# Optimization experiments

Hardware: AMD Instinct MI355X
Metric: run time of the kernel (lower is better)

The kernel has to match this reference:

```python
import jax, jax.numpy as jnp
import numpy as np

DIM, HEADS, WS = 256, 16, 8
B, H, W = 2, 252, 252
BN_EPS = 1e-5


def _rel_index():
    # Same construction as the torch buffer relative_position_index (64,64)
    coords = np.stack(np.meshgrid(np.arange(WS), np.arange(WS), indexing='ij'))
    flat = coords.reshape(2, -1)
    rel = (flat[:, :, None] - flat[:, None, :]).transpose(1, 2, 0).copy()
    rel[..., 0] += WS - 1
    rel[..., 1] += WS - 1
    rel[..., 0] *= 2 * WS - 1
    return jnp.asarray(rel.sum(-1))

REL_IDX = _rel_index()  # (WS*WS, WS*WS) int


def _conv(x, w, pad, groups=1):
    return jax.lax.conv_general_dilated(
        x, w, (1, 1), [(pad[0], pad[0]), (pad[1], pad[1])],
        dimension_numbers=('NCHW', 'OIHW', 'NCHW'), feature_group_count=groups)


def setup_inputs() -> dict:
    key = jax.random.key(0)
    ks = jax.random.split(key, 8)
    s = lambda k, shape, sc: jax.random.normal(k, shape, jnp.float32) * sc
    z = lambda: jnp.zeros((DIM,), jnp.float32)
    return {
        'x': s(ks[0], (B, DIM, H, W), 1.0),
        'w_qkv': s(ks[1], (3 * DIM, DIM, 1, 1), 0.05),
        'rel_bias_table': s(ks[2], ((2 * WS - 1) ** 2, HEADS), 0.02),
        'w_h': s(ks[3], (DIM, DIM, WS, 1), 0.02),
        'b_h': z(),
        'w_v': s(ks[4], (DIM, DIM, 1, WS), 0.02),
        'b_v': z(),
        'w_dw': s(ks[5], (DIM, 1, WS, WS), 0.05),
        'bn_gamma': jnp.ones((DIM,), jnp.float32),
        'bn_beta': z(),
        'bn_mean': z(),
        'bn_var': jnp.ones((DIM,), jnp.float32),
        'w_pw': s(ks[6], (DIM, DIM, 1, 1), 0.05),
    }


def reference(x, w_qkv, rel_bias_table, w_h, b_h, w_v, b_v, w_dw,
              bn_gamma, bn_beta, bn_mean, bn_var, w_pw):
    Bc, C, Hc, Wc = x.shape
    pad_h, pad_w = WS - Hc % WS, WS - Wc % WS
    xp = jnp.pad(x, ((0, 0), (0, 0), (0, pad_h), (0, pad_w)), mode='reflect')
    Hp, Wp = Hc + pad_h, Wc + pad_w
    hh, ww, d = Hp // WS, Wp // WS, C // HEADS

    qkv = _conv(xp, w_qkv, (0, 0))  # (B, 3C, Hp, Wp)
    # b (qkv h d) (hh ws1) (ww ws2) -> qkv (b hh ww) h (ws1 ws2) d
    qkv = qkv.reshape(Bc, 3, HEADS, d, hh, WS, ww, WS)
    qkv = qkv.transpose(1, 0, 4, 6, 2, 5, 7, 3).reshape(3, Bc * hh * ww, HEADS, WS * WS, d)
    q, k, v = qkv[0], qkv[1], qkv[2]

    dots = jnp.einsum('nhid,nhjd->nhij', q, k) * (d ** -0.5)
    bias = rel_bias_table[REL_IDX.reshape(-1)].reshape(WS * WS, WS * WS, HEADS)
    dots = dots + bias.transpose(2, 0, 1)[None]  # (1, h, 64, 64)
    attn = jax.nn.softmax(dots, axis=-1)
    out = jnp.einsum('nhij,nhjd->nhid', attn, v)
    # (b hh ww) h (ws1 ws2) d -> b (h d) (hh ws1) (ww ws2)
    out = out.reshape(Bc, hh, ww, HEADS, WS, WS, d)
    out = out.transpose(0, 3, 6, 1, 4, 2, 5).reshape(Bc, C, Hp, Wp)
    out = out[:, :, :Hc, :Wc]

    p1 = _conv(jnp.pad(out, ((0, 0), (0, 0), (0, 1), (0, 0)), mode='reflect'),
               w_h, (WS // 2 - 1, 0)) + b_h[None, :, None, None]
    p2 = _conv(jnp.pad(out, ((0, 0), (0, 0), (0, 0), (0, 1)), mode='reflect'),
               w_v, (0, WS // 2 - 1)) + b_v[None, :, None, None]
    y = jnp.pad(p1 + p2, ((0, 0), (0, 0), (0, 1), (0, 1)), mode='reflect')
    y = _conv(y, w_dw, ((WS - 1) // 2, (WS - 1) // 2), groups=DIM)  # depthwise
    inv = bn_gamma / jnp.sqrt(bn_var + BN_EPS)
    y = y * inv[None, :, None, None] + (bn_beta - bn_mean * inv)[None, :, None, None]
    y = _conv(y, w_pw, (0, 0))  # pointwise 1x1
    return y[:, :, :Hc, :Wc]
```

## Files before the change

### kernel.cpp

```cpp
#include <hip/hip_runtime.h>
#include <hip/hip_bf16.h>

#define HC 252
#define WC 252
#define CD 256
#define NHEADS 16

#define XP_W 264
#define XP_ROW (XP_W*256)
#define XP_BH  (252*XP_ROW)

typedef unsigned short u16;
typedef unsigned int u32;
typedef __attribute__((ext_vector_type(8))) short bf16x8;
typedef __attribute__((ext_vector_type(4))) float f32x4;
typedef __attribute__((ext_vector_type(4))) u32 u32x4;
typedef __attribute__((ext_vector_type(2))) u32 u32x2;

#define XP_BYTES (2u * 2u * (unsigned)XP_BH)
#define ZP_OFF   XP_BYTES
#define ZP_BYTES 409600u
#define WT_OFF   (ZP_OFF + ZP_BYTES)
#define WT_ELEMS (128*8192)
#define WPW_OFF  (WT_OFF + (unsigned)WT_ELEMS*2u)
#define WPW_ELEMS (8*8192)
#define WQ_OFF   (WPW_OFF + (unsigned)WPW_ELEMS*2u)
#define WQ_ELEMS (768*256)
#define BIAS_OFF (WQ_OFF + (unsigned)WQ_ELEMS*2u)

__device__ __forceinline__ u16 bfu(float f) {
    __hip_bfloat16 h = __float2bfloat16(f);
    return *(reinterpret_cast<u16*>(&h));
}
__device__ __forceinline__ u32 pack2(float a, float b) {
    return (u32)bfu(a) | ((u32)bfu(b) << 16);
}
__device__ __forceinline__ float bf2f(u16 v) {
    union { u32 u; float f; } cv; cv.u = ((u32)v) << 16; return cv.f;
}

__global__ __launch_bounds__(256, 2) void attn_mfma(
    const float* __restrict__ x, const u16* __restrict__ WQ,
    const float* __restrict__ BIASF, u16* __restrict__ xp)
{
    __shared__ __align__(16) char smem[73728];

    const int bid = blockIdx.x;
    const int zz = (bid & 7) * 256 + (bid >> 3);
    const int wx = zz & 31, wy = (zz >> 5) & 31, b = zz >> 10;
    const int tid = threadIdx.x;
    const int lane = tid & 63, wid = tid >> 6;
    const int g = lane >> 4, li = lane & 15;

    {
        int ci = tid;
        const float* srcc = x + (size_t)(b * 256 + ci) * (HC * WC);
        #pragma unroll
        for (int r = 0; r < 8; ++r) {
            int h = wy * 8 + r; if (h >= HC) h = 2 * HC - 2 - h;
            const float* src = srcc + h * WC;
            float v[8];
            if (wx == 31) {
                #pragma unroll
                for (int c = 0; c < 8; ++c) {
                    int w = 248 + c; if (w >= WC) w = 2 * WC - 2 - w;
                    v[c] = src[w];
                }
            } else {
                float4 f0 = *(const float4*)(src + wx * 8);
                float4 f1 = *(const float4*)(src + wx * 8 + 4);
                v[0]=f0.x; v[1]=f0.y; v[2]=f0.z; v[3]=f0.w;
                v[4]=f1.x; v[5]=f1.y; v[6]=f1.z; v[7]=f1.w;
            }
            #pragma unroll
            for (int c = 0; c < 8; ++c) {
                int pos = r * 8 + c;
                int byte = pos * 512 + ((ci * 2) ^ ((pos & 7) << 4));
                *(u16*)(smem + byte) = bfu(v[c]);
            }
        }
    }
    __syncthreads();

    const int WB = 32768 + wid * 10240;
    char* Qb = smem + WB;
    char* Kb = smem + WB + 2048;
    char* Vb = smem + WB + 4096;
    char* Pb = smem + WB + 6144;

    const bf16x8 zf = {0,0,0,0,0,0,0,0};

    #pragma unroll 1
    for (int hh = 0; hh < 4; ++hh) {
        const int head = wid * 4 + hh;

        f32x4 acc[3][4];
        #pragma unroll
        for (int p = 0; p < 3; ++p)
            #pragma unroll
            for (int nf = 0; nf < 4; ++nf) acc[p][nf] = (f32x4){0.f,0.f,0.f,0.f};

        for (int ks = 0; ks < 8; ++ks) {
            bf16x8 bx[4];
            #pragma unroll
            for (int nf = 0; nf < 4; ++nf) {
                int pos = 16 * nf + li;
                int byte = pos * 512 + ((ks * 64 + 16 * g) ^ ((pos & 7) << 4));
                bx[nf] = *(const bf16x8*)(smem + byte);
            }
            bf16x8 aw[3];
            #pragma unroll
            for (int p = 0; p < 3; ++p) {
                int o = p * 256 + head * 16 + li;
                aw[p] = *(const bf16x8*)(WQ + o * 256 + ks * 32 + 8 * g);
            }
            __builtin_amdgcn_s_setprio(1);
            #pragma unroll
            for (int p = 0; p < 3; ++p)
                #pragma unroll
                for (int nf = 0; nf < 4; ++nf)
                    acc[p][nf] = __builtin_amdgcn_mfma_f32_16x16x32_bf16(aw[p], bx[nf], acc[p][nf], 0, 0, 0);
            __builtin_amdgcn_s_setprio(0);
        }

        #pragma unroll
        for (int p = 0; p < 3; ++p) {
            if (p < 2) {
                char* base = (p == 0) ? Qb : Kb;
                #pragma unroll
                for (int nf = 0; nf < 4; ++nf) {
                    int pos = 16 * nf + li;
                    u32 lo = pack2(acc[p][nf][0], acc[p][nf][1]);
                    u32 hi = pack2(acc[p][nf][2], acc[p][nf][3]);
                    int byte = pos * 32 + ((8 * g) ^ (((pos >> 2) & 1) << 4));
                    *(u32x2*)(base + byte) = (u32x2){lo, hi};
                }
            } else {
                #pragma unroll
                for (int nf = 0; nf < 4; ++nf) {
                    int pos = 16 * nf + li;
                    #pragma unroll
                    for (int r = 0; r < 4; ++r) {
                        int d = 4 * g + r;
                        int byte = (pos >> 3) * 256 + d * 16 + (pos & 7) * 2;
                        *(u16*)(Vb + byte) = bfu(acc[p][nf][r]);
                    }
                }
            }
        }

        f32x4 s[4][4];
        #pragma unroll
        for (int mf = 0; mf < 4; ++mf)
            #pragma unroll
            for (int nf = 0; nf < 4; ++nf) s[mf][nf] = (f32x4){0.f,0.f,0.f,0.f};
        bf16x8 bk[4];
        #pragma unroll
        for (int nf = 0; nf < 4; ++nf) {
            int pos = 16 * nf + li;
            bk[nf] = (g < 2) ? *(const bf16x8*)(Kb + pos * 32 + ((16 * g) ^ (((pos >> 2) & 1) << 4))) : zf;
        }
        __builtin_amdgcn_s_setprio(1);
        #pragma unroll
        for (int mf = 0; mf < 4; ++mf) {
            int pos = 16 * mf + li;
            bf16x8 aq = (g < 2) ? *(const bf16x8*)(Qb + pos * 32 + ((16 * g) ^ (((pos >> 2) & 1) << 4))) : zf;
            #pragma unroll
            for (int nf = 0; nf < 4; ++nf)
                s[mf][nf] = __builtin_amdgcn_mfma_f32_16x16x32_bf16(aq, bk[nf], s[mf][nf], 0, 0, 0);
        }
        __builtin_amdgcn_s_setprio(0);

        f32x4 e[4][4];
        f32x4 rs[4];
        #pragma unroll
        for (int mf = 0; mf < 4; ++mf) rs[mf] = (f32x4){0.f,0.f,0.f,0.f};
        #pragma unroll
        for (int mf = 0; mf < 4; ++mf)
            #pragma unroll
            for (int nf = 0; nf < 4; ++nf) {
                f32x4 b4 = *(const f32x4*)(BIASF + (((head * 4 + mf) * 4 + nf) * 64 + lane) * 4);
                #pragma unroll
                for (int r = 0; r < 4; ++r) {
                    float ev = __expf(s[mf][nf][r] * 0.25f + b4[r]);
                    e[mf][nf][r] = ev;
                    rs[mf][r] += ev;
                }
            }
        #pragma unroll
        for (int mf = 0; mf < 4; ++mf)
            #pragma unroll
            for (int r = 0; r < 4; ++r) {
                float t = rs[mf][r];
                t += __shfl_xor(t, 1); t += __shfl_xor(t, 2);
                t += __shfl_xor(t, 4); t += __shfl_xor(t, 8);
                rs[mf][r] = t;
            }

        f32x4 o[4];
        #pragma unroll
        for (int mf = 0; mf < 4; ++mf) o[mf] = (f32x4){0.f,0.f,0.f,0.f};
        const bool even = !(lane & 1);
        #pragma unroll
        for (int hf = 0; hf < 2; ++hf) {
            #pragma unroll
            for (int mf = 0; mf < 4; ++mf)
                #pragma unroll
                for (int nfl = 0; nfl < 2; ++nfl) {
                    f32x4 ee = e[mf][2 * hf + nfl];
                    float p0 = __shfl_xor(ee[0], 1), p1 = __shfl_xor(ee[1], 1);
                    float p2 = __shfl_xor(ee[2], 1), p3 = __shfl_xor(ee[3], 1);
                    int jl = 16 * nfl + (li & ~1);
                    u32 w0, w1; int r0;
                    if (even) { w0 = pack2(ee[0], p0); w1 = pack2(ee[1], p1); r0 = 0; }
                    else      { w0 = pack2(p2, ee[2]); w1 = pack2(p3, ee[3]); r0 = 2; }
                    int i0 = 16 * mf + 4 * g + r0, i1 = i0 + 1;
                    *(u32*)(Pb + i0 * 64 + ((2 * jl) ^ ((i0 & 3) << 4))) = w0;
                    *(u32*)(Pb + i1 * 64 + ((2 * jl) ^ ((i1 & 3) << 4))) = w1;
                }
            bf16x8 bv = *(const bf16x8*)(Vb + (4 * hf + g) * 256 + li * 16);
            __builtin_amdgcn_s_setprio(1);
            #pragma unroll
            for (int mf = 0; mf < 4; ++mf) {
                int i = 16 * mf + li;
                bf16x8 ap = *(const bf16x8*)(Pb + i * 64 + ((16 * g) ^ ((i & 3) << 4)));
                o[mf] = __builtin_amdgcn_mfma_f32_16x16x32_bf16(ap, bv, o[mf], 0, 0, 0);
            }
            __builtin_amdgcn_s_setprio(0);
        }

        #pragma unroll
        for (int mf = 0; mf < 4; ++mf) {
            int h = wy * 8 + 2 * mf + (g >> 1);
            int wbase = wx * 8 + 4 * (g & 1);
            if (h < HC && wbase < WC) {
                size_t rowb = ((size_t)(b * HC + h)) * XP_ROW + (size_t)(head * 16 + li);
                #pragma unroll
                for (int r = 0; r < 4; ++r) {
                    float v = o[mf][r] / rs[mf][r];
                    xp[rowb + (size_t)(wbase + r + 4) * 256] = bfu(v);
                }
            }
        }
    }
}

__global__ __launch_bounds__(256) void wprep_kernel(
    const float* __restrict__ wh, const float* __restrict__ wv,
    const float* __restrict__ wpw, const float* __restrict__ wqkv,
    const float* __restrict__ btab, u16* __restrict__ wsu)
{
    int i = blockIdx.x * 256 + threadIdx.x;
    u16* WT = wsu + WT_OFF / 2;
    u16* WP = wsu + WPW_OFF / 2;
    u16* ZP = wsu + ZP_OFF / 2;
    u16* WQp = wsu + WQ_OFF / 2;
    float* BF = (float*)(wsu + BIAS_OFF / 2);
    if (i < WT_ELEMS) {
        int j = i & 7, l = (i >> 3) & 1023, s = i >> 13;
        int kb = (l >> 8) & 3;
        int co = (l & 255) ^ (kb << 1);
        float v;
        if (s < 64) {
            int t = s >> 3, ci = (s & 7) * 32 + kb * 8 + j;
            v = wh[co * 2048 + ci * 8 + t];
        } else {
            int s2 = s - 64;
            int t = s2 >> 3, ci = (s2 & 7) * 32 + kb * 8 + j;
            v = wv[co * 2048 + ci * 8 + t];
        }
        WT[i] = bfu(v);
    } else if (i < WT_ELEMS + WPW_ELEMS) {
        int i2 = i - WT_ELEMS;
        int j = i2 & 7, l = (i2 >> 3) & 1023, s = i2 >> 13;
        int kb = (l >> 8) & 3;
        int co = (l & 255) ^ (kb << 1);
        WP[i2] = bfu(wpw[co * 256 + s * 32 + kb * 8 + j]);
    } else if (i < WT_ELEMS + WPW_ELEMS + (int)(ZP_BYTES / 2)) {
        ZP[i - WT_ELEMS - WPW_ELEMS] = 0;
    } else if (i < WT_ELEMS + WPW_ELEMS + (int)(ZP_BYTES / 2) + WQ_ELEMS) {
        int i4 = i - WT_ELEMS - WPW_ELEMS - (int)(ZP_BYTES / 2);
        WQp[i4] = bfu(wqkv[i4]);
    } else {
        int i5 = i - WT_ELEMS - WPW_ELEMS - (int)(ZP_BYTES / 2) - WQ_ELEMS;
        if (i5 < 16384) {
            int lane = i5 & 63, nf = (i5 >> 6) & 3, mf = (i5 >> 8) & 3, head = i5 >> 10;
            int gg = lane >> 4, ll = lane & 15;
            #pragma unroll
            for (int r = 0; r < 4; ++r) {
                int row = 16 * mf + 4 * gg + r;
                int col = 16 * nf + ll;
                int dy = (row >> 3) - (col >> 3) + 7;
                int dx = (row & 7) - (col & 7) + 7;
                BF[i5 * 4 + r] = btab[(dy * 15 + dx) * NHEADS + head];
            }
        }
    }
}

__global__ __launch_bounds__(256) void halo_kernel(u16* __restrict__ xp)
{
    int i = blockIdx.x * 256 + threadIdx.x;
    if (i >= 2 * 252 * 12 * 256) return;
    int ci = i & 255;
    int c12 = (i >> 8) % 12;
    int row = i / (12 * 256);
    int wp = (c12 < 4) ? c12 : 252 + c12;
    u16 v = 0;
    if (wp == 256) v = xp[(size_t)row * XP_ROW + 254 * 256 + ci];
    xp[(size_t)row * XP_ROW + (size_t)wp * 256 + ci] = v;
}

__global__ __launch_bounds__(512, 2) void sepconv_mfma(
    const u16* __restrict__ xpt, const u16* __restrict__ WT,
    const u16* __restrict__ ZP,
    const float* __restrict__ b_h, const float* __restrict__ b_v,
    u16* __restrict__ P)
{
    __shared__ __align__(16) u16 As[2][8192];
    __shared__ __align__(16) u16 Bs[2][256 * 36];

    const int bid = blockIdx.x;
    const int zz = (bid & 7) * 63 + (bid >> 3);
    const int h = zz % HC, b = zz / HC;
    const int tid = threadIdx.x;
    const int lane = tid & 63, wid = tid >> 6;
    const int wr = wid >> 2, wc = wid & 3;
    const int cq = lane & 15, kb = lane >> 4;

    const int wB = tid & 255;
    const int oc0 = tid >> 8;
    const int tb = (wB + 4) * 256 + oc0 * 8;
    const int bsw = wB * 36 + oc0 * 8;

    const u16* const xb = xpt + (size_t)(b * HC) * XP_ROW;

    f32x4 acc[8][4];
    #pragma unroll
    for (int m = 0; m < 8; ++m)
        #pragma unroll
        for (int n = 0; n < 4; ++n) acc[m][n] = (f32x4){0.f, 0.f, 0.f, 0.f};

    u32x4 rA[2];
    u32x4 rB0, rB1;

#define SC_SRC(t, RP, SO)                                                      \
    if ((t) < 64) {                                                            \
        int tt = (t) >> 3;                                                     \
        int jt = h + tt - 3;                                                   \
        int jr = (jt == 252) ? 250 : jt;                                       \
        RP = (jt >= 0 && jt <= 252) ? (xpt + ((size_t)(b * HC) + jr) * XP_ROW) : ZP; \
        SO = ((t) & 7) * 32;                                                   \
    } else {                                                                   \
        int tt = ((t) - 64) >> 3;                                              \
        RP = xb + (size_t)h * XP_ROW + (tt - 3) * 256;                         \
        SO = (((t) - 64) & 7) * 32;                                            \
    }

    rA[0] = *(const u32x4*)(WT + (size_t)tid * 8);
    rA[1] = *(const u32x4*)(WT + (size_t)(512 + tid) * 8);
    {
        const u16* rp; int so;
        SC_SRC(0, rp, so)
        rB0 = *(const u32x4*)(rp + so + tb);
        rB1 = *(const u32x4*)(rp + so + tb + 16);
    }
    *(u32x4*)&As[0][(size_t)tid * 8] = rA[0];
    *(u32x4*)&As[0][(size_t)(512 + tid) * 8] = rA[1];
    *(u32x4*)&Bs[0][bsw] = rB0;
    *(u32x4*)&Bs[0][bsw + 16] = rB1;

    #pragma unroll 1
    for (int s = 0; s < 128; ++s) {
        const int cur = s & 1;
        const int s1 = s + 1;
        if (s1 < 128) {
            rA[0] = *(const u32x4*)(WT + (size_t)s1 * 8192 + (size_t)tid * 8);
            rA[1] = *(const u32x4*)(WT + (size_t)s1 * 8192 + (size_t)(512 + tid) * 8);
            const u16* rp; int so;
            SC_SRC(s1, rp, so)
            rB0 = *(const u32x4*)(rp + so + tb);
            rB1 = *(const u32x4*)(rp + so + tb + 16);
        }
        __syncthreads();

        {
            bf16x8 af[8], bfr[4];
            #pragma unroll
            for (int m = 0; m < 8; ++m) {
                int row = wr * 128 + m * 16 + cq;
                af[m] = *(const bf16x8*)&As[cur][(kb * 256 + (row ^ (kb << 1))) * 8];
            }
            #pragma unroll
            for (int n = 0; n < 4; ++n)
                bfr[n] = *(const bf16x8*)&Bs[cur][(wc * 64 + n * 16 + cq) * 36 + kb * 8];
            __builtin_amdgcn_s_setprio(1);
            #pragma unroll
            for (int m = 0; m < 8; ++m)
                #pragma unroll
                for (int n = 0; n < 4; ++n)
                    acc[m][n] = __builtin_amdgcn_mfma_f32_16x16x32_bf16(af[m], bfr[n], acc[m][n], 0, 0, 0);
            __builtin_amdgcn_s_setprio(0);
        }

        if (s1 < 128) {
            const int nxt = cur ^ 1;
            *(u32x4*)&As[nxt][(size_t)tid * 8] = rA[0];
            *(u32x4*)&As[nxt][(size_t)(512 + tid) * 8] = rA[1];
            *(u32x4*)&Bs[nxt][bsw] = rB0;
            *(u32x4*)&Bs[nxt][bsw + 16] = rB1;
        }
    }
#undef SC_SRC

    const int rq = lane >> 4, cc = lane & 15;
    #pragma unroll
    for (int m = 0; m < 8; ++m) {
        int cgb = wr * 128 + m * 16 + rq * 4;
        float bias[4];
        #pragma unroll
        for (int rr = 0; rr < 4; ++rr) bias[rr] = b_h[cgb + rr] + b_v[cgb + rr];
        #pragma unroll
        for (int n = 0; n < 4; ++n) {
            int wg = wc * 64 + n * 16 + cc;
            if (wg < WC) {
                #pragma unroll
                for (int rr = 0; rr < 4; ++rr)
                    P[((size_t)(b * CD + cgb + rr) * HC + h) * WC + wg] = bfu(acc[m][n][rr] + bias[rr]);
            }
        }
    }
}

__global__ __launch_bounds__(256) void dwbn_kernel(
    const u16* __restrict__ P, const float* __restrict__ w_dw,
    const float* __restrict__ gamma, const float* __restrict__ beta,
    const float* __restrict__ mean, const float* __restrict__ var,
    __hip_bfloat16* __restrict__ Yb)
{
    __shared__ float ps[15][42];
    __shared__ float wd[64];
    const int bw = blockIdx.x, bh = blockIdx.y, bz = blockIdx.z;
    const int b = bz >> 8, c = bz & 255;
    const int h0 = bh * 8, w0 = bw * 32;
    const int tid = threadIdx.x;
    if (tid < 64) wd[tid] = w_dw[c * 64 + tid];
    for (int it = 0; it < 3; ++it) {
        int flat = tid + it * 256;
        if (flat < 630) {
            int row = flat / 42, col = flat % 42;
            int j = h0 - 3 + row, wcol = w0 - 3 + col;
            float v = 0.f;
            if (j >= 0 && j <= HC && wcol >= 0 && wcol <= WC) {
                int jr = (j == HC) ? (HC - 2) : j;
                int wr2 = (wcol == WC) ? (WC - 2) : wcol;
                v = bf2f(P[((size_t)(b * CD + c) * HC + jr) * WC + wr2]);
            }
            ps[row][col] = v;
        }
    }
    __syncthreads();
    const int r = tid >> 5, cc = tid & 31;
    const int h = h0 + r, w = w0 + cc;
    if (h < HC && w < WC) {
        float s = 0.f;
        #pragma unroll
        for (int u = 0; u < 8; ++u)
            #pragma unroll
            for (int v2 = 0; v2 < 8; ++v2)
                s += wd[u * 8 + v2] * ps[r + u][cc + v2];
        const float inv = gamma[c] * rsqrtf(var[c] + 1e-5f);
        Yb[((b * CD + c) * HC + h) * WC + w] = __float2bfloat16(s * inv + (beta[c] - mean[c] * inv));
    }
}

__global__ __launch_bounds__(512, 2) void pw_mfma(
    const u16* __restrict__ Y, const u16* __restrict__ WP,
    float* __restrict__ O)
{
    __shared__ __align__(16) u16 As[2][8192];
    __shared__ __align__(16) u16 Bs[2][256 * 36];

    const int bid = blockIdx.x;
    const int zz = (bid & 7) * 63 + (bid >> 3);
    const int h = zz % HC, b = zz / HC;
    const int tid = threadIdx.x;
    const int lane = tid & 63, wid = tid >> 6;
    const int wr = wid >> 2, wc = wid & 3;
    const int cq = lane & 15, kb = lane >> 4;

    const int wl2 = (tid & 127) * 2;
    const int oc = tid >> 7;

    const u16* yb = Y + ((size_t)(b * 256 + oc * 8) * HC + h) * WC + wl2;

    const int bw0 = wl2 * 36 + oc * 8;
    const int bw1 = bw0 + 36;

    f32x4 acc[8][4];
    #pragma unroll
    for (int m = 0; m < 8; ++m)
        #pragma unroll
        for (int n = 0; n < 4; ++n) acc[m][n] = (f32x4){0.f, 0.f, 0.f, 0.f};

    u32x4 rA[2];
    u32 rB[8];

    rA[0] = *(const u32x4*)(WP + (size_t)tid * 8);
    rA[1] = *(const u32x4*)(WP + (size_t)(512 + tid) * 8);
    #pragma unroll
    for (int j = 0; j < 8; ++j)
        rB[j] = *(const u32*)(yb + (size_t)j * (HC * WC));
    *(u32x4*)&As[0][(size_t)tid * 8] = rA[0];
    *(u32x4*)&As[0][(size_t)(512 + tid) * 8] = rA[1];
    {
        union { bf16x8 v; u32 u[4]; } p0, p1;
        #pragma unroll
        for (int q = 0; q < 4; ++q) {
            p0.u[q] = __builtin_amdgcn_perm(rB[2 * q + 1], rB[2 * q], 0x05040100u);
            p1.u[q] = __builtin_amdgcn_perm(rB[2 * q + 1], rB[2 * q], 0x07060302u);
        }
        *(bf16x8*)&Bs[0][bw0] = p0.v;
        *(bf16x8*)&Bs[0][bw1] = p1.v;
    }

    #pragma unroll 1
    for (int s = 0; s < 8; ++s) {
        const int cur = s & 1;
        const int s1 = s + 1;
        if (s1 < 8) {
            rA[0] = *(const u32x4*)(WP + (size_t)s1 * 8192 + (size_t)tid * 8);
            rA[1] = *(const u32x4*)(WP + (size_t)s1 * 8192 + (size_t)(512 + tid) * 8);
            #pragma unroll
            for (int j = 0; j < 8; ++j)
                rB[j] = *(const u32*)(yb + (size_t)(s1 * 32 + j) * (HC * WC));
        }
        __syncthreads();

        {
            bf16x8 af[8], bfr[4];
            #pragma unroll
            for (int m = 0; m < 8; ++m) {
                int row = wr * 128 + m * 16 + cq;
                af[m] = *(const bf16x8*)&As[cur][(kb * 256 + (row ^ (kb << 1))) * 8];
            }
            #pragma unroll
            for (int n = 0; n < 4; ++n)
                bfr[n] = *(const bf16x8*)&Bs[cur][(wc * 64 + n * 16 + cq) * 36 + kb * 8];
            __builtin_amdgcn_s_setprio(1);
            #pragma unroll
            for (int m = 0; m < 8; ++m)
                #pragma unroll
                for (int n = 0; n < 4; ++n)
                    acc[m][n] = __builtin_amdgcn_mfma_f32_16x16x32_bf16(af[m], bfr[n], acc[m][n], 0, 0, 0);
            __builtin_amdgcn_s_setprio(0);
        }

        if (s1 < 8) {
            const int nxt = cur ^ 1;
            *(u32x4*)&As[nxt][(size_t)tid * 8] = rA[0];
            *(u32x4*)&As[nxt][(size_t)(512 + tid) * 8] = rA[1];
            union { bf16x8 v; u32 u[4]; } p0, p1;
            #pragma unroll
            for (int q = 0; q < 4; ++q) {
                p0.u[q] = __builtin_amdgcn_perm(rB[2 * q + 1], rB[2 * q], 0x05040100u);
                p1.u[q] = __builtin_amdgcn_perm(rB[2 * q + 1], rB[2 * q], 0x07060302u);
            }
            *(bf16x8*)&Bs[nxt][bw0] = p0.v;
            *(bf16x8*)&Bs[nxt][bw1] = p1.v;
        }
    }

    const int rq = lane >> 4, cc = lane & 15;
    #pragma unroll
    for (int m = 0; m < 8; ++m) {
        int cgb = wr * 128 + m * 16 + rq * 4;
        #pragma unroll
        for (int n = 0; n < 4; ++n) {
            int wg = wc * 64 + n * 16 + cc;
            if (wg < WC) {
                #pragma unroll
                for (int rr = 0; rr < 4; ++rr)
                    O[((size_t)(b * CD + cgb + rr) * HC + h) * WC + wg] = acc[m][n][rr];
            }
        }
    }
}

extern "C" void kernel_launch(void* const* d_in, const int* in_sizes, int n_in,
                              void* d_out, int out_size, void* d_ws, size_t ws_size,
                              hipStream_t stream)
{
    const float* x      = (const float*)d_in[0];
    const float* w_qkv  = (const float*)d_in[1];
    const float* bias_t = (const float*)d_in[2];
    const float* w_h    = (const float*)d_in[3];
    const float* b_h    = (const float*)d_in[4];
    const float* w_v    = (const float*)d_in[5];
    const float* b_v    = (const float*)d_in[6];
    const float* w_dw   = (const float*)d_in[7];
    const float* bn_g   = (const float*)d_in[8];
    const float* bn_b   = (const float*)d_in[9];
    const float* bn_m   = (const float*)d_in[10];
    const float* bn_v   = (const float*)d_in[11];
    const float* w_pw   = (const float*)d_in[12];
    float* out = (float*)d_out;

    u16* wsu = (u16*)d_ws;
    const u16* XPu = wsu;
    const u16* ZPu = wsu + ZP_OFF / 2;
    const u16* WTu = wsu + WT_OFF / 2;
    const u16* WPu = wsu + WPW_OFF / 2;
    const u16* WQu = wsu + WQ_OFF / 2;
    const float* BFu = (const float*)(wsu + BIAS_OFF / 2);

    wprep_kernel<<<5984, 256, 0, stream>>>(w_h, w_v, w_pw, w_qkv, bias_t, wsu);
    attn_mfma<<<2048, 256, 0, stream>>>(x, WQu, BFu, wsu);
    halo_kernel<<<6048, 256, 0, stream>>>(wsu);
    sepconv_mfma<<<504, 512, 0, stream>>>(XPu, WTu, ZPu, b_h, b_v, (u16*)d_out);
    dwbn_kernel<<<dim3(8, 32, 512), 256, 0, stream>>>((const u16*)d_out, w_dw, bn_g, bn_b,
                                                      bn_m, bn_v, (__hip_bfloat16*)d_ws);
    pw_mfma<<<504, 512, 0, stream>>>(wsu, WPu, out);
}
```

Measured before the change: 689.6 us.

## Software-pipeline QKV projection, enlarge depthwise tiles, stage pointwise output through LDS

The attention kernel now computes the next head's QKV projection while the current head's softmax and PV run, and drops the setprio hints. The depthwise+BN kernel handles 16x64 tiles with four outputs per thread and writes packed bf16 pairs, so halo loads are reused across more outputs and global stores are wider. The pointwise kernel transposes its accumulators through LDS so each lane writes float4 rows instead of scattered scalar stores. Together these target latency hiding and memory-store efficiency, at the cost of higher register pressure in the attention kernel (an extra 12 f32x4 accumulators) and an extra LDS round trip in the pointwise epilogue.

```diff
diff --git a/kernel.cpp b/kernel.cpp
--- a/kernel.cpp
+++ b/kernel.cpp
@@ -12,6 +12,7 @@
 
 typedef unsigned short u16;
 typedef unsigned int u32;
+typedef __attribute__((ext_vector_type(4))) u16 u16x4;
 typedef __attribute__((ext_vector_type(8))) short bf16x8;
 typedef __attribute__((ext_vector_type(4))) float f32x4;
 typedef __attribute__((ext_vector_type(4))) u32 u32x4;
@@ -90,39 +91,36 @@
 
     const bf16x8 zf = {0,0,0,0,0,0,0,0};
 
+#define QKV_LOOP(ACC, HEADV)                                                  \
+    for (int ks = 0; ks < 8; ++ks) {                                          \
+        bf16x8 bx[4];                                                         \
+        _Pragma("unroll") for (int nf = 0; nf < 4; ++nf) {                    \
+            int pos = 16 * nf + li;                                           \
+            int byte = pos * 512 + ((ks * 64 + 16 * g) ^ ((pos & 7) << 4));   \
+            bx[nf] = *(const bf16x8*)(smem + byte);                           \
+        }                                                                     \
+        bf16x8 aw[3];                                                         \
+        _Pragma("unroll") for (int p = 0; p < 3; ++p) {                       \
+            int o = p * 256 + (HEADV) * 16 + li;                              \
+            aw[p] = *(const bf16x8*)(WQ + o * 256 + ks * 32 + 8 * g);         \
+        }                                                                     \
+        _Pragma("unroll") for (int p = 0; p < 3; ++p) {                       \
+            _Pragma("unroll") for (int nf = 0; nf < 4; ++nf)                  \
+                ACC[p][nf] = __builtin_amdgcn_mfma_f32_16x16x32_bf16(aw[p], bx[nf], ACC[p][nf], 0, 0, 0); \
+        }                                                                     \
+    }
+
+    f32x4 accA[3][4], accN[3][4];
+    #pragma unroll
+    for (int p = 0; p < 3; ++p)
+        #pragma unroll
+        for (int nf = 0; nf < 4; ++nf) accA[p][nf] = (f32x4){0.f,0.f,0.f,0.f};
+    QKV_LOOP(accA, wid * 4)
+
     #pragma unroll 1
     for (int hh = 0; hh < 4; ++hh) {
         const int head = wid * 4 + hh;
 
-        f32x4 acc[3][4];
-        #pragma unroll
-        for (int p = 0; p < 3; ++p)
-            #pragma unroll
-            for (int nf = 0; nf < 4; ++nf) acc[p][nf] = (f32x4){0.f,0.f,0.f,0.f};
-
-        for (int ks = 0; ks < 8; ++ks) {
-            bf16x8 bx[4];
-            #pragma unroll
-            for (int nf = 0; nf < 4; ++nf) {
-                int pos = 16 * nf + li;
-                int byte = pos * 512 + ((ks * 64 + 16 * g) ^ ((pos & 7) << 4));
-                bx[nf] = *(const bf16x8*)(smem + byte);
-            }
-            bf16x8 aw[3];
-            #pragma unroll
-            for (int p = 0; p < 3; ++p) {
-                int o = p * 256 + head * 16 + li;
-                aw[p] = *(const bf16x8*)(WQ + o * 256 + ks * 32 + 8 * g);
-            }
-            __builtin_amdgcn_s_setprio(1);
-            #pragma unroll
-            for (int p = 0; p < 3; ++p)
-                #pragma unroll
-                for (int nf = 0; nf < 4; ++nf)
-                    acc[p][nf] = __builtin_amdgcn_mfma_f32_16x16x32_bf16(aw[p], bx[nf], acc[p][nf], 0, 0, 0);
-            __builtin_amdgcn_s_setprio(0);
-        }
-
         #pragma unroll
         for (int p = 0; p < 3; ++p) {
             if (p < 2) {
@@ -130,8 +128,8 @@
                 #pragma unroll
                 for (int nf = 0; nf < 4; ++nf) {
                     int pos = 16 * nf + li;
-                    u32 lo = pack2(acc[p][nf][0], acc[p][nf][1]);
-                    u32 hi = pack2(acc[p][nf][2], acc[p][nf][3]);
+                    u32 lo = pack2(accA[p][nf][0], accA[p][nf][1]);
+                    u32 hi = pack2(accA[p][nf][2], accA[p][nf][3]);
                     int byte = pos * 32 + ((8 * g) ^ (((pos >> 2) & 1) << 4));
                     *(u32x2*)(base + byte) = (u32x2){lo, hi};
                 }
@@ -143,7 +141,7 @@
                     for (int r = 0; r < 4; ++r) {
                         int d = 4 * g + r;
                         int byte = (pos >> 3) * 256 + d * 16 + (pos & 7) * 2;
-                        *(u16*)(Vb + byte) = bfu(acc[p][nf][r]);
+                        *(u16*)(Vb + byte) = bfu(accA[p][nf][r]);
                     }
                 }
             }
@@ -170,6 +168,14 @@
                 s[mf][nf] = __builtin_amdgcn_mfma_f32_16x16x32_bf16(aq, bk[nf], s[mf][nf], 0, 0, 0);
         }
         __builtin_amdgcn_s_setprio(0);
+
+        if (hh < 3) {
+            #pragma unroll
+            for (int p = 0; p < 3; ++p)
+                #pragma unroll
+                for (int nf = 0; nf < 4; ++nf) accN[p][nf] = (f32x4){0.f,0.f,0.f,0.f};
+            QKV_LOOP(accN, head + 1)
+        }
 
         f32x4 e[4][4];
         f32x4 rs[4];
@@ -242,7 +248,15 @@
                 }
             }
         }
-    }
+
+        if (hh < 3) {
+            #pragma unroll
+            for (int p = 0; p < 3; ++p)
+                #pragma unroll
+                for (int nf = 0; nf < 4; ++nf) accA[p][nf] = accN[p][nf];
+        }
+    }
+#undef QKV_LOOP
 }
 
 __global__ __launch_bounds__(256) void wprep_kernel(
@@ -438,17 +452,17 @@
     const float* __restrict__ mean, const float* __restrict__ var,
     __hip_bfloat16* __restrict__ Yb)
 {
-    __shared__ float ps[15][42];
+    __shared__ float ps[23][73];
     __shared__ float wd[64];
     const int bw = blockIdx.x, bh = blockIdx.y, bz = blockIdx.z;
     const int b = bz >> 8, c = bz & 255;
-    const int h0 = bh * 8, w0 = bw * 32;
+    const int h0 = bh * 16, w0 = bw * 64;
     const int tid = threadIdx.x;
     if (tid < 64) wd[tid] = w_dw[c * 64 + tid];
-    for (int it = 0; it < 3; ++it) {
+    for (int it = 0; it < 7; ++it) {
         int flat = tid + it * 256;
-        if (flat < 630) {
-            int row = flat / 42, col = flat % 42;
+        if (flat < 23 * 71) {
+            int row = flat / 71, col = flat % 71;
             int j = h0 - 3 + row, wcol = w0 - 3 + col;
             float v = 0.f;
             if (j >= 0 && j <= HC && wcol >= 0 && wcol <= WC) {
@@ -460,17 +474,26 @@
         }
     }
     __syncthreads();
-    const int r = tid >> 5, cc = tid & 31;
-    const int h = h0 + r, w = w0 + cc;
+    const int r = tid >> 4;
+    const int c0 = (tid & 15) * 4;
+    const int h = h0 + r, w = w0 + c0;
     if (h < HC && w < WC) {
-        float s = 0.f;
+        float s0 = 0.f, s1 = 0.f, s2 = 0.f, s3 = 0.f;
         #pragma unroll
         for (int u = 0; u < 8; ++u)
             #pragma unroll
-            for (int v2 = 0; v2 < 8; ++v2)
-                s += wd[u * 8 + v2] * ps[r + u][cc + v2];
+            for (int v2 = 0; v2 < 8; ++v2) {
+                const float wv = wd[u * 8 + v2];
+                const float* pr = &ps[r + u][c0 + v2];
+                s0 += wv * pr[0]; s1 += wv * pr[1];
+                s2 += wv * pr[2]; s3 += wv * pr[3];
+            }
         const float inv = gamma[c] * rsqrtf(var[c] + 1e-5f);
-        Yb[((b * CD + c) * HC + h) * WC + w] = __float2bfloat16(s * inv + (beta[c] - mean[c] * inv));
+        const float sh = beta[c] - mean[c] * inv;
+        u32x2 pk;
+        pk[0] = pack2(s0 * inv + sh, s1 * inv + sh);
+        pk[1] = pack2(s2 * inv + sh, s3 * inv + sh);
+        *(u32x2*)&Yb[((size_t)(b * CD + c) * HC + h) * WC + w] = pk;
     }
 }
 
@@ -571,17 +594,26 @@
         }
     }
 
-    const int rq = lane >> 4, cc = lane & 15;
+    __syncthreads();
+    float* tsl = (float*)&Bs[0][0] + wid * (16 * 68);
+    const int rq = lane >> 4;
+    const int r2 = lane >> 2;
+    const int wq = (lane & 3) * 16;
     #pragma unroll
     for (int m = 0; m < 8; ++m) {
-        int cgb = wr * 128 + m * 16 + rq * 4;
-        #pragma unroll
-        for (int n = 0; n < 4; ++n) {
-            int wg = wc * 64 + n * 16 + cc;
-            if (wg < WC) {
-                #pragma unroll
-                for (int rr = 0; rr < 4; ++rr)
-                    O[((size_t)(b * CD + cgb + rr) * HC + h) * WC + wg] = acc[m][n][rr];
+        #pragma unroll
+        for (int n = 0; n < 4; ++n)
+            #pragma unroll
+            for (int rr = 0; rr < 4; ++rr)
+                tsl[(rq * 4 + rr) * 68 + n * 16 + cq] = acc[m][n][rr];
+        const int co = wr * 128 + m * 16 + r2;
+        float* orow = O + ((size_t)(b * CD + co) * HC + h) * WC + wc * 64;
+        #pragma unroll
+        for (int q = 0; q < 4; ++q) {
+            int wl = wq + 4 * q;
+            if (wc * 64 + wl < WC) {
+                f32x4 v4 = *(const f32x4*)&tsl[r2 * 68 + wl];
+                *(f32x4*)&orow[wl] = v4;
             }
         }
     }
@@ -618,7 +650,7 @@
     attn_mfma<<<2048, 256, 0, stream>>>(x, WQu, BFu, wsu);
     halo_kernel<<<6048, 256, 0, stream>>>(wsu);
     sepconv_mfma<<<504, 512, 0, stream>>>(XPu, WTu, ZPu, b_h, b_v, (u16*)d_out);
-    dwbn_kernel<<<dim3(8, 32, 512), 256, 0, stream>>>((const u16*)d_out, w_dw, bn_g, bn_b,
+    dwbn_kernel<<<dim3(4, 16, 512), 256, 0, stream>>>((const u16*)d_out, w_dw, bn_g, bn_b,
                                                       bn_m, bn_v, (__hip_bfloat16*)d_ws);
     pw_mfma<<<504, 512, 0, stream>>>(wsu, WPu, out);
 }
```

Result: slower. 711.3 us (+3.2%).
